# Performance work log

Measured on AMD Instinct MI355X. Metric: run time of the kernel, lower is better.

## Reference

```python
import jax, jax.numpy as jnp
import numpy as np

B, S, N, D, H = 4, 1024, 1024, 1024, 16
HD = D // H
EPS = 1e-5


def _xavier(key, shape):
    fan_in, fan_out = shape[1], shape[0]
    a = (6.0 / (fan_in + fan_out)) ** 0.5
    return jax.random.uniform(key, shape, jnp.float32, -a, a)


def layer_norm(x, g, b):
    m = jnp.mean(x, axis=-1, keepdims=True)
    v = jnp.mean(jnp.square(x - m), axis=-1, keepdims=True)
    return (x - m) * jax.lax.rsqrt(v + EPS) * g + b


def setup_inputs() -> dict:
    key = jax.random.key(0)
    ks = jax.random.split(key, 8)
    return {
        "x_q": jax.random.normal(ks[0], (B, S, D), jnp.float32),
        "x_k": jax.random.normal(ks[1], (B, N, D), jnp.float32),
        "x_v": jax.random.normal(ks[2], (B, N, D), jnp.float32),
        "Wq": _xavier(ks[3], (D, D)),
        "Wk": _xavier(ks[4], (D, D)),
        "Wv": _xavier(ks[5], (D, D)),
        "Wp": _xavier(ks[6], (D, D)),
        "qn_g": jnp.ones((HD,), jnp.float32),
        "qn_b": jnp.zeros((HD,), jnp.float32),
        "kn_g": jnp.ones((HD,), jnp.float32),
        "kn_b": jnp.zeros((HD,), jnp.float32),
        "on_g": jnp.ones((D,), jnp.float32),
        "on_b": jnp.zeros((D,), jnp.float32),
    }


def reference(x_q, x_k, x_v, Wq, Wk, Wv, Wp, qn_g, qn_b, kn_g, kn_b, on_g, on_b):
    scale = HD ** (-0.5)
    q = jnp.einsum('bsd,ed->bse', x_q, Wq)  # torch Linear: x @ W.T
    k = jnp.einsum('bnd,ed->bne', x_k, Wk)
    v = jnp.einsum('bnd,ed->bne', x_v, Wv)
    # Faithful to original: q is reshaped WITHOUT transpose (B,H,S,HD)
    q = q.reshape(B, H, S, HD)
    k = k.reshape(B, N, H, HD).transpose(0, 2, 1, 3)  # (B,H,N,HD)
    v = v.reshape(B, N, H, HD).transpose(0, 2, 1, 3)  # (B,H,N,HD)
    q = layer_norm(q, qn_g, qn_b) * scale
    k = layer_norm(k, kn_g, kn_b)
    attn = jax.nn.softmax(jnp.einsum('bhsd,bhnd->bhsn', q, k), axis=-1)
    x = jnp.einsum('bhsn,bhnd->bhsd', attn, v)
    x = x.transpose(0, 2, 1, 3).reshape(B, S, D)
    x = layer_norm(x, on_g, on_b)
    return jnp.einsum('bsd,ed->bse', x, Wp)
```

## Files before the change

kernel.cpp:

```cpp
#include <hip/hip_runtime.h>
#include <cstdint>

typedef unsigned short u16;
typedef __attribute__((ext_vector_type(4))) float f32x4;
typedef __attribute__((ext_vector_type(8))) short bf16x8;

__device__ __forceinline__ u16 f2bf(float f) {
  uint32_t u = __builtin_bit_cast(uint32_t, f);
  u += 0x7FFFu + ((u >> 16) & 1u);
  return (u16)(u >> 16);
}

__device__ __forceinline__ void gld16(const void* g, void* l) {
  __builtin_amdgcn_global_load_lds((const __attribute__((address_space(1))) void*)g,
                                   (__attribute__((address_space(3))) void*)l,
                                   16, 0, 0);
}

__global__ __launch_bounds__(256) void cast_all(const float* __restrict__ xq, const float* __restrict__ xk,
                                                const float* __restrict__ xv, const float* __restrict__ Wq,
                                                const float* __restrict__ Wk, const float* __restrict__ Wv,
                                                const float* __restrict__ Wp,
                                                u16* __restrict__ oq, u16* __restrict__ ok, u16* __restrict__ ov,
                                                u16* __restrict__ owq, u16* __restrict__ owk,
                                                u16* __restrict__ owv, u16* __restrict__ owp) {
  int bid = blockIdx.x;
  const float* src; u16* dst; size_t i;
  if (bid < 12288) {
    const int p = bid >> 12, ib = bid & 4095;
    src = (p == 0) ? xq : ((p == 1) ? xk : xv);
    dst = (p == 0) ? oq : ((p == 1) ? ok : ov);
    i = (size_t)ib * 256 + threadIdx.x;
  } else {
    bid -= 12288;
    const int p = bid >> 10, ib = bid & 1023;
    src = (p == 0) ? Wq : ((p == 1) ? Wk : ((p == 2) ? Wv : Wp));
    dst = (p == 0) ? owq : ((p == 1) ? owk : ((p == 2) ? owv : owp));
    i = (size_t)ib * 256 + threadIdx.x;
  }
  float4 v = *(const float4*)(src + i * 4);
  uint2 pk;
  pk.x = (uint32_t)f2bf(v.x) | ((uint32_t)f2bf(v.y) << 16);
  pk.y = (uint32_t)f2bf(v.z) | ((uint32_t)f2bf(v.w) << 16);
  *(uint2*)(dst + i * 4) = pk;
}

__device__ __forceinline__ void gemm_mainloop(const u16* __restrict__ A, const u16* __restrict__ B,
                                              int bm, int bn, u16* Al, u16* Bl,
                                              f32x4 (&acc)[4][4]) {
  const int t = threadIdx.x;
  const int w = t >> 6;
  const int lane = t & 63;
  const int l15 = lane & 15, l4 = lane >> 4;
  const int wr = w >> 1, wc = w & 1;

  const u16* Ab = A + (size_t)bm * 128 * 1024;
  const u16* Bb = B + (size_t)bn * 128 * 1024;

  for (int kt = 0; kt < 1024; kt += 64) {
#pragma unroll
    for (int p = 0; p < 4; ++p) {
      const int idx = p * 256 + t;
      const int row = idx >> 3, ch = idx & 7;
      const int sch = ch ^ (row & 7);
      gld16(Ab + (size_t)row * 1024 + kt + sch * 8, (char*)Al + p * 4096 + (w << 10));
      gld16(Bb + (size_t)row * 1024 + kt + sch * 8, (char*)Bl + p * 4096 + (w << 10));
    }
    __syncthreads();
#pragma unroll
    for (int ks = 0; ks < 2; ++ks) {
      bf16x8 af[4], bfr[4];
#pragma unroll
      for (int mi = 0; mi < 4; ++mi) {
        const int row = wr * 64 + mi * 16 + l15;
        const int ch = (ks * 4 + l4) ^ (row & 7);
        af[mi] = *(const bf16x8*)&Al[row * 64 + ch * 8];
      }
#pragma unroll
      for (int nj = 0; nj < 4; ++nj) {
        const int row = wc * 64 + nj * 16 + l15;
        const int ch = (ks * 4 + l4) ^ (row & 7);
        bfr[nj] = *(const bf16x8*)&Bl[row * 64 + ch * 8];
      }
#pragma unroll
      for (int mi = 0; mi < 4; ++mi)
#pragma unroll
        for (int nj = 0; nj < 4; ++nj)
          acc[mi][nj] = __builtin_amdgcn_mfma_f32_16x16x32_bf16(af[mi], bfr[nj], acc[mi][nj], 0, 0, 0);
    }
    __syncthreads();
  }
}

__global__ __launch_bounds__(256) void gemm_qkv(const u16* __restrict__ A0, const u16* __restrict__ A1,
                                                const u16* __restrict__ A2, const u16* __restrict__ B0,
                                                const u16* __restrict__ B1, const u16* __restrict__ B2,
                                                u16* __restrict__ Qout, u16* __restrict__ Kout,
                                                u16* __restrict__ Vout,
                                                const float* __restrict__ qg, const float* __restrict__ qb,
                                                const float* __restrict__ kg, const float* __restrict__ kb) {
  __shared__ __align__(16) u16 Al[128 * 64];
  __shared__ __align__(16) u16 Bl[128 * 64];
  const int p = blockIdx.x >> 8;
  const int b0 = blockIdx.x & 255;
  const int bid = ((b0 & 7) << 5) + (b0 >> 3);
  const int bm = bid >> 3, bn = bid & 7;
  const u16* A = (p == 0) ? A0 : ((p == 1) ? A1 : A2);
  const u16* B = (p == 0) ? B0 : ((p == 1) ? B1 : B2);

  f32x4 acc[4][4];
#pragma unroll
  for (int i = 0; i < 4; ++i)
#pragma unroll
    for (int j = 0; j < 4; ++j) acc[i][j] = (f32x4){0.f, 0.f, 0.f, 0.f};

  gemm_mainloop(A, B, bm, bn, Al, Bl, acc);

  const int t = threadIdx.x, w = t >> 6, lane = t & 63;
  const int l15 = lane & 15, l4 = lane >> 4;
  const int wr = w >> 1, wc = w & 1;
  const int c = bn * 2 + wc;

  if (p == 2) {
#pragma unroll
    for (int mi = 0; mi < 4; ++mi) {
      const int n0 = bm * 128 + wr * 64 + mi * 16 + l4 * 4;
      const int bi = n0 >> 10, ni = n0 & 1023;
      const int nt = ni >> 6, ng = (ni >> 3) & 7, no = ni & 7;
#pragma unroll
      for (int nj = 0; nj < 4; ++nj) {
        const int hd = nj * 16 + l15;
        uint32_t w0 = (uint32_t)f2bf(acc[mi][nj][0]) | ((uint32_t)f2bf(acc[mi][nj][1]) << 16);
        uint32_t w1 = (uint32_t)f2bf(acc[mi][nj][2]) | ((uint32_t)f2bf(acc[mi][nj][3]) << 16);
        uint2 pk = {w0, w1};
        const size_t addr = ((size_t)(bi * 16 + c) * 64 + hd) * 1024 + nt * 64 + ((ng ^ (hd & 7)) << 3) + no;
        *(uint2*)(Vout + addr) = pk;
      }
    }
    return;
  }

  const float scale = (p == 0) ? 0.18033688011112042f : 1.0f;
  const float* gv = (p == 0) ? qg : kg;
  const float* bv = (p == 0) ? qb : kb;
  u16* out = (p == 0) ? Qout : Kout;
  float gl[4], blc[4];
#pragma unroll
  for (int nj = 0; nj < 4; ++nj) {
    gl[nj] = gv[nj * 16 + l15];
    blc[nj] = bv[nj * 16 + l15] * scale;
  }
#pragma unroll
  for (int mi = 0; mi < 4; ++mi) {
#pragma unroll
    for (int r = 0; r < 4; ++r) {
      float s1 = 0.f, s2 = 0.f;
#pragma unroll
      for (int nj = 0; nj < 4; ++nj) {
        const float x = acc[mi][nj][r];
        s1 += x; s2 += x * x;
      }
#pragma unroll
      for (int mk = 1; mk < 16; mk <<= 1) {
        s1 += __shfl_xor(s1, mk, 64);
        s2 += __shfl_xor(s2, mk, 64);
      }
      const float mean = s1 * (1.0f / 64.0f);
      const float var = s2 * (1.0f / 64.0f) - mean * mean;
      const float rr = rsqrtf(var + 1e-5f) * scale;
      const int row_g = bm * 128 + wr * 64 + mi * 16 + l4 * 4 + r;
      const int bi = row_g >> 10, rsi = row_g & 1023;
      size_t base; int sw;
      if (p == 0) {
        const int h = rsi >> 6;
        const int s2i = ((rsi & 63) << 4) + c;
        base = ((size_t)(bi * 16 + h) * 1024 + s2i) * 64;
        sw = (s2i & 7) << 3;
      } else {
        base = ((size_t)(bi * 16 + c) * 1024 + rsi) * 64;
        sw = (rsi & 7) << 3;
      }
#pragma unroll
      for (int nj = 0; nj < 4; ++nj) {
        const float y = (acc[mi][nj][r] - mean) * rr * gl[nj] + blc[nj];
        out[base + ((nj * 16 + l15) ^ sw)] = f2bf(y);
      }
    }
  }
}

__global__ __launch_bounds__(256) void gemm_p(const u16* __restrict__ A, const u16* __restrict__ B,
                                              float* __restrict__ C) {
  __shared__ __align__(16) u16 Al[128 * 64];
  __shared__ __align__(16) u16 Bl[128 * 64];
  const int bid = ((blockIdx.x & 7) << 5) + (blockIdx.x >> 3);
  const int bm = bid >> 3, bn = bid & 7;

  f32x4 acc[4][4];
#pragma unroll
  for (int i = 0; i < 4; ++i)
#pragma unroll
    for (int j = 0; j < 4; ++j) acc[i][j] = (f32x4){0.f, 0.f, 0.f, 0.f};

  gemm_mainloop(A, B, bm, bn, Al, Bl, acc);

  const int t = threadIdx.x, w = t >> 6, lane = t & 63;
  const int l15 = lane & 15, l4 = lane >> 4;
  const int wr = w >> 1, wc = w & 1;
  float* Cb = C + (size_t)bm * 128 * 1024 + bn * 128;
#pragma unroll
  for (int mi = 0; mi < 4; ++mi)
#pragma unroll
    for (int nj = 0; nj < 4; ++nj) {
      const int row = wr * 64 + mi * 16 + l4 * 4;
      const int col = wc * 64 + nj * 16 + l15;
#pragma unroll
      for (int r = 0; r < 4; ++r)
        Cb[(size_t)(row + r) * 1024 + col] = acc[mi][nj][r];
    }
}

__global__ __launch_bounds__(256) void flash(const u16* __restrict__ Q,
                                             const u16* __restrict__ Km,
                                             const u16* __restrict__ Vt,
                                             float* __restrict__ ctx) {
  __shared__ __align__(16) u16 Kl[2 * 64 * 64];
  __shared__ __align__(16) u16 Vl[2 * 64 * 64];
  __shared__ __align__(16) u16 Pl[64 * 64];
  const int bid = ((blockIdx.x & 7) << 7) + (blockIdx.x >> 3);
  const int bh = bid >> 4, qt = bid & 15;
  const int t = threadIdx.x, w = t >> 6, lane = t & 63;
  const int l15 = lane & 15, l4 = lane >> 4;
  const int sx = (l15 & 7) << 3;
  const int ea0 = (l4 * 8) ^ sx;
  const int ea1 = ea0 ^ 32;

  const u16* Qrow = Q + ((size_t)bh * 1024 + qt * 64 + w * 16 + l15) * 64;
  const bf16x8 aq0 = *(const bf16x8*)(Qrow + ea0);
  const bf16x8 aq1 = *(const bf16x8*)(Qrow + ea1);
  const bf16x8 vone = {0x3F80, 0x3F80, 0x3F80, 0x3F80, 0x3F80, 0x3F80, 0x3F80, 0x3F80};

  const u16* Kg = Km + (size_t)bh * 65536;
  const u16* Vg = Vt + (size_t)bh * 65536;

  gld16((const char*)Kg + t * 16, (char*)Kl + (w << 10));
  gld16((const char*)Kg + 4096 + t * 16, (char*)Kl + 4096 + (w << 10));
  gld16(Vg + (t >> 3) * 1024 + (t & 7) * 8, (char*)Vl + (w << 10));
  gld16(Vg + ((t + 256) >> 3) * 1024 + (t & 7) * 8, (char*)Vl + 4096 + (w << 10));
  __syncthreads();

  f32x4 o[4];
  for (int i = 0; i < 4; ++i) o[i] = (f32x4){0.f, 0.f, 0.f, 0.f};
  f32x4 o4 = (f32x4){0.f, 0.f, 0.f, 0.f};

  int cur = 0;
  for (int nt2 = 0; nt2 < 16; ++nt2) {
    if (nt2 < 15) {
      const int nb = (cur ^ 1) * 8192;
      const char* ksrc = (const char*)(Kg + (size_t)(nt2 + 1) * 4096);
      gld16(ksrc + t * 16, (char*)Kl + nb + (w << 10));
      gld16(ksrc + 4096 + t * 16, (char*)Kl + nb + 4096 + (w << 10));
      gld16(Vg + (t >> 3) * 1024 + (nt2 + 1) * 64 + (t & 7) * 8, (char*)Vl + nb + (w << 10));
      gld16(Vg + ((t + 256) >> 3) * 1024 + (nt2 + 1) * 64 + (t & 7) * 8, (char*)Vl + nb + 4096 + (w << 10));
    }
    const u16* Kc = Kl + cur * 4096;
    const u16* Vc = Vl + cur * 4096;

    f32x4 sc[4];
    for (int cj = 0; cj < 4; ++cj) sc[cj] = (f32x4){0.f, 0.f, 0.f, 0.f};
#pragma unroll
    for (int ks = 0; ks < 2; ++ks) {
      const int ea = ks ? ea1 : ea0;
      const bf16x8 aq = ks ? aq1 : aq0;
#pragma unroll
      for (int cj = 0; cj < 4; ++cj) {
        bf16x8 bk = *(const bf16x8*)&Kc[(cj * 16 + l15) * 64 + ea];
        sc[cj] = __builtin_amdgcn_mfma_f32_16x16x32_bf16(aq, bk, sc[cj], 0, 0, 0);
      }
    }

#pragma unroll
    for (int cj = 0; cj < 4; ++cj)
#pragma unroll
      for (int r = 0; r < 4; ++r) {
        const float pf = __builtin_amdgcn_exp2f(sc[cj][r]);
        const uint32_t u = __builtin_bit_cast(uint32_t, pf);
        const int prow = w * 16 + l4 * 4 + r;
        Pl[prow * 64 + ((cj * 16 + l15) ^ (((l4 * 4 + r) & 7) << 3))] = (u16)((u + 0x8000u) >> 16);
      }

#pragma unroll
    for (int ks = 0; ks < 2; ++ks) {
      const int ea = ks ? ea1 : ea0;
      bf16x8 ap = *(const bf16x8*)&Pl[(w * 16 + l15) * 64 + ea];
#pragma unroll
      for (int c2 = 0; c2 < 4; ++c2) {
        bf16x8 bv = *(const bf16x8*)&Vc[(c2 * 16 + l15) * 64 + ea];
        o[c2] = __builtin_amdgcn_mfma_f32_16x16x32_bf16(ap, bv, o[c2], 0, 0, 0);
      }
      o4 = __builtin_amdgcn_mfma_f32_16x16x32_bf16(ap, vone, o4, 0, 0, 0);
    }
    __syncthreads();
    cur ^= 1;
  }

  const int b = bh >> 4, h = bh & 15;
#pragma unroll
  for (int c2 = 0; c2 < 4; ++c2) {
#pragma unroll
    for (int r = 0; r < 4; ++r) {
      const int s2 = qt * 64 + w * 16 + l4 * 4 + r;
      const int hd = c2 * 16 + l15;
      ctx[((size_t)b * 1024 + s2) * 1024 + h * 64 + hd] = o[c2][r] / o4[r];
    }
  }
}

__global__ __launch_bounds__(256) void ln_row(const float* __restrict__ X,
                                              const float* __restrict__ g,
                                              const float* __restrict__ bb,
                                              u16* __restrict__ out) {
  __shared__ float red[8];
  const int row = blockIdx.x, t = threadIdx.x;
  const int w = t >> 6, lane = t & 63;
  const float* xr = X + (size_t)row * 1024;
  float4 v = *(const float4*)(xr + t * 4);
  float s = v.x + v.y + v.z + v.w;
  for (int mk = 1; mk < 64; mk <<= 1) s += __shfl_xor(s, mk, 64);
  if (lane == 0) red[w] = s;
  __syncthreads();
  const float mean = (red[0] + red[1] + red[2] + red[3]) * (1.0f / 1024.0f);
  const float dx = v.x - mean, dy = v.y - mean, dz = v.z - mean, dw = v.w - mean;
  float q = dx * dx + dy * dy + dz * dz + dw * dw;
  for (int mk = 1; mk < 64; mk <<= 1) q += __shfl_xor(q, mk, 64);
  if (lane == 0) red[4 + w] = q;
  __syncthreads();
  const float var = (red[4] + red[5] + red[6] + red[7]) * (1.0f / 1024.0f);
  const float rs = rsqrtf(var + 1e-5f);
  float4 gg = *(const float4*)(g + t * 4);
  float4 b4 = *(const float4*)(bb + t * 4);
  uint2 pk;
  pk.x = (uint32_t)f2bf(dx * rs * gg.x + b4.x) | ((uint32_t)f2bf(dy * rs * gg.y + b4.y) << 16);
  pk.y = (uint32_t)f2bf(dz * rs * gg.z + b4.z) | ((uint32_t)f2bf(dw * rs * gg.w + b4.w) << 16);
  *(uint2*)(out + (size_t)row * 1024 + t * 4) = pk;
}

extern "C" void kernel_launch(void* const* d_in, const int* in_sizes, int n_in,
                              void* d_out, int out_size, void* d_ws, size_t ws_size,
                              hipStream_t stream) {
  (void)in_sizes; (void)n_in; (void)out_size; (void)ws_size;
  const float* x_q = (const float*)d_in[0];
  const float* x_k = (const float*)d_in[1];
  const float* x_v = (const float*)d_in[2];
  const float* Wq  = (const float*)d_in[3];
  const float* Wk  = (const float*)d_in[4];
  const float* Wv  = (const float*)d_in[5];
  const float* Wp  = (const float*)d_in[6];
  const float* qn_g = (const float*)d_in[7];
  const float* qn_b = (const float*)d_in[8];
  const float* kn_g = (const float*)d_in[9];
  const float* kn_b = (const float*)d_in[10];
  const float* on_g = (const float*)d_in[11];
  const float* on_b = (const float*)d_in[12];

  char* ws = (char*)d_ws;
  u16* xq_bf = (u16*)(ws + (0ull << 20));
  u16* xk_bf = (u16*)(ws + (8ull << 20));
  u16* xv_bf = (u16*)(ws + (16ull << 20));
  u16* Wq_bf = (u16*)(ws + (24ull << 20));
  u16* Wk_bf = (u16*)(ws + (26ull << 20));
  u16* Wv_bf = (u16*)(ws + (28ull << 20));
  u16* Wp_bf = (u16*)(ws + (30ull << 20));
  u16* Qa   = (u16*)(ws + (32ull << 20));
  u16* Ka   = (u16*)(ws + (40ull << 20));
  u16* Vtb  = (u16*)(ws + (48ull << 20));
  float* ctxf = (float*)(ws + (56ull << 20));
  u16* ctxb = (u16*)(ws + (72ull << 20));

  cast_all<<<16384, 256, 0, stream>>>(x_q, x_k, x_v, Wq, Wk, Wv, Wp,
                                      xq_bf, xk_bf, xv_bf, Wq_bf, Wk_bf, Wv_bf, Wp_bf);

  gemm_qkv<<<768, 256, 0, stream>>>(xq_bf, xk_bf, xv_bf, Wq_bf, Wk_bf, Wv_bf,
                                    Qa, Ka, Vtb, qn_g, qn_b, kn_g, kn_b);
  flash<<<1024, 256, 0, stream>>>(Qa, Ka, Vtb, ctxf);
  ln_row<<<4096, 256, 0, stream>>>(ctxf, on_g, on_b, ctxb);
  gemm_p<<<256, 256, 0, stream>>>(ctxb, Wp_bf, (float*)d_out);
}
```

Measured before the change: 126.9 us.

## Double-buffer GEMM K-loop in half tiles and process two query tiles per flash block

```diff
diff --git a/kernel.cpp b/kernel.cpp
--- a/kernel.cpp
+++ b/kernel.cpp
@@ -56,39 +56,60 @@
 
   const u16* Ab = A + (size_t)bm * 128 * 1024;
   const u16* Bb = B + (size_t)bn * 128 * 1024;
-
-  for (int kt = 0; kt < 1024; kt += 64) {
-#pragma unroll
-    for (int p = 0; p < 4; ++p) {
-      const int idx = p * 256 + t;
-      const int row = idx >> 3, ch = idx & 7;
-      const int sch = ch ^ (row & 7);
-      gld16(Ab + (size_t)row * 1024 + kt + sch * 8, (char*)Al + p * 4096 + (w << 10));
-      gld16(Bb + (size_t)row * 1024 + kt + sch * 8, (char*)Bl + p * 4096 + (w << 10));
-    }
-    __syncthreads();
-#pragma unroll
-    for (int ks = 0; ks < 2; ++ks) {
+  const int r0 = t >> 2, c0 = (t & 3) * 8;
+  const int r1 = r0 + 64;
+  const int wb = w << 10;
+
+  gld16(Ab + (size_t)r0 * 1024 + c0, (char*)Al + wb);
+  gld16(Ab + (size_t)r1 * 1024 + c0, (char*)Al + 4096 + wb);
+  gld16(Bb + (size_t)r0 * 1024 + c0, (char*)Bl + wb);
+  gld16(Bb + (size_t)r1 * 1024 + c0, (char*)Bl + 4096 + wb);
+  __syncthreads();
+
+#pragma unroll 1
+  for (int it = 0; it < 16; ++it) {
+    {
+      const int ktn = it * 64 + 32;
+      gld16(Ab + (size_t)r0 * 1024 + ktn + c0, (char*)Al + 8192 + wb);
+      gld16(Ab + (size_t)r1 * 1024 + ktn + c0, (char*)Al + 8192 + 4096 + wb);
+      gld16(Bb + (size_t)r0 * 1024 + ktn + c0, (char*)Bl + 8192 + wb);
+      gld16(Bb + (size_t)r1 * 1024 + ktn + c0, (char*)Bl + 8192 + 4096 + wb);
       bf16x8 af[4], bfr[4];
 #pragma unroll
-      for (int mi = 0; mi < 4; ++mi) {
-        const int row = wr * 64 + mi * 16 + l15;
-        const int ch = (ks * 4 + l4) ^ (row & 7);
-        af[mi] = *(const bf16x8*)&Al[row * 64 + ch * 8];
-      }
-#pragma unroll
-      for (int nj = 0; nj < 4; ++nj) {
-        const int row = wc * 64 + nj * 16 + l15;
-        const int ch = (ks * 4 + l4) ^ (row & 7);
-        bfr[nj] = *(const bf16x8*)&Bl[row * 64 + ch * 8];
-      }
+      for (int mi = 0; mi < 4; ++mi)
+        af[mi] = *(const bf16x8*)&Al[(wr * 64 + mi * 16 + l15) * 32 + l4 * 8];
+#pragma unroll
+      for (int nj = 0; nj < 4; ++nj)
+        bfr[nj] = *(const bf16x8*)&Bl[(wc * 64 + nj * 16 + l15) * 32 + l4 * 8];
 #pragma unroll
       for (int mi = 0; mi < 4; ++mi)
 #pragma unroll
         for (int nj = 0; nj < 4; ++nj)
           acc[mi][nj] = __builtin_amdgcn_mfma_f32_16x16x32_bf16(af[mi], bfr[nj], acc[mi][nj], 0, 0, 0);
-    }
-    __syncthreads();
+      __syncthreads();
+    }
+    {
+      const int ktn = it * 64 + 64;
+      if (ktn < 1024) {
+        gld16(Ab + (size_t)r0 * 1024 + ktn + c0, (char*)Al + wb);
+        gld16(Ab + (size_t)r1 * 1024 + ktn + c0, (char*)Al + 4096 + wb);
+        gld16(Bb + (size_t)r0 * 1024 + ktn + c0, (char*)Bl + wb);
+        gld16(Bb + (size_t)r1 * 1024 + ktn + c0, (char*)Bl + 4096 + wb);
+      }
+      bf16x8 af[4], bfr[4];
+#pragma unroll
+      for (int mi = 0; mi < 4; ++mi)
+        af[mi] = *(const bf16x8*)&Al[4096 + (wr * 64 + mi * 16 + l15) * 32 + l4 * 8];
+#pragma unroll
+      for (int nj = 0; nj < 4; ++nj)
+        bfr[nj] = *(const bf16x8*)&Bl[4096 + (wc * 64 + nj * 16 + l15) * 32 + l4 * 8];
+#pragma unroll
+      for (int mi = 0; mi < 4; ++mi)
+#pragma unroll
+        for (int nj = 0; nj < 4; ++nj)
+          acc[mi][nj] = __builtin_amdgcn_mfma_f32_16x16x32_bf16(af[mi], bfr[nj], acc[mi][nj], 0, 0, 0);
+      __syncthreads();
+    }
   }
 }
 
@@ -99,8 +120,8 @@
                                                 u16* __restrict__ Vout,
                                                 const float* __restrict__ qg, const float* __restrict__ qb,
                                                 const float* __restrict__ kg, const float* __restrict__ kb) {
-  __shared__ __align__(16) u16 Al[128 * 64];
-  __shared__ __align__(16) u16 Bl[128 * 64];
+  __shared__ __align__(16) u16 Al[2 * 128 * 32];
+  __shared__ __align__(16) u16 Bl[2 * 128 * 32];
   const int p = blockIdx.x >> 8;
   const int b0 = blockIdx.x & 255;
   const int bid = ((b0 & 7) << 5) + (b0 >> 3);
@@ -191,8 +212,8 @@
 
 __global__ __launch_bounds__(256) void gemm_p(const u16* __restrict__ A, const u16* __restrict__ B,
                                               float* __restrict__ C) {
-  __shared__ __align__(16) u16 Al[128 * 64];
-  __shared__ __align__(16) u16 Bl[128 * 64];
+  __shared__ __align__(16) u16 Al[2 * 128 * 32];
+  __shared__ __align__(16) u16 Bl[2 * 128 * 32];
   const int bid = ((blockIdx.x & 7) << 5) + (blockIdx.x >> 3);
   const int bm = bid >> 3, bn = bid & 7;
 
@@ -226,18 +247,20 @@
                                              float* __restrict__ ctx) {
   __shared__ __align__(16) u16 Kl[2 * 64 * 64];
   __shared__ __align__(16) u16 Vl[2 * 64 * 64];
-  __shared__ __align__(16) u16 Pl[64 * 64];
-  const int bid = ((blockIdx.x & 7) << 7) + (blockIdx.x >> 3);
-  const int bh = bid >> 4, qt = bid & 15;
+  __shared__ __align__(16) u16 Pl[2 * 64 * 64];
+  const int bid = ((blockIdx.x & 7) << 6) + (blockIdx.x >> 3);
+  const int bh = bid >> 3, qt2 = bid & 7;
   const int t = threadIdx.x, w = t >> 6, lane = t & 63;
   const int l15 = lane & 15, l4 = lane >> 4;
   const int sx = (l15 & 7) << 3;
   const int ea0 = (l4 * 8) ^ sx;
   const int ea1 = ea0 ^ 32;
 
-  const u16* Qrow = Q + ((size_t)bh * 1024 + qt * 64 + w * 16 + l15) * 64;
-  const bf16x8 aq0 = *(const bf16x8*)(Qrow + ea0);
-  const bf16x8 aq1 = *(const bf16x8*)(Qrow + ea1);
+  const u16* Qrow = Q + ((size_t)bh * 1024 + qt2 * 128 + w * 16 + l15) * 64;
+  const bf16x8 aq00 = *(const bf16x8*)(Qrow + ea0);
+  const bf16x8 aq01 = *(const bf16x8*)(Qrow + ea1);
+  const bf16x8 aq10 = *(const bf16x8*)(Qrow + 4096 + ea0);
+  const bf16x8 aq11 = *(const bf16x8*)(Qrow + 4096 + ea1);
   const bf16x8 vone = {0x3F80, 0x3F80, 0x3F80, 0x3F80, 0x3F80, 0x3F80, 0x3F80, 0x3F80};
 
   const u16* Kg = Km + (size_t)bh * 65536;
@@ -249,9 +272,13 @@
   gld16(Vg + ((t + 256) >> 3) * 1024 + (t & 7) * 8, (char*)Vl + 4096 + (w << 10));
   __syncthreads();
 
-  f32x4 o[4];
-  for (int i = 0; i < 4; ++i) o[i] = (f32x4){0.f, 0.f, 0.f, 0.f};
-  f32x4 o4 = (f32x4){0.f, 0.f, 0.f, 0.f};
+  f32x4 o[2][4];
+  f32x4 o4[2];
+#pragma unroll
+  for (int s = 0; s < 2; ++s) {
+    for (int i = 0; i < 4; ++i) o[s][i] = (f32x4){0.f, 0.f, 0.f, 0.f};
+    o4[s] = (f32x4){0.f, 0.f, 0.f, 0.f};
+  }
 
   int cur = 0;
   for (int nt2 = 0; nt2 < 16; ++nt2) {
@@ -266,39 +293,46 @@
     const u16* Kc = Kl + cur * 4096;
     const u16* Vc = Vl + cur * 4096;
 
-    f32x4 sc[4];
-    for (int cj = 0; cj < 4; ++cj) sc[cj] = (f32x4){0.f, 0.f, 0.f, 0.f};
-#pragma unroll
-    for (int ks = 0; ks < 2; ++ks) {
-      const int ea = ks ? ea1 : ea0;
-      const bf16x8 aq = ks ? aq1 : aq0;
-#pragma unroll
-      for (int cj = 0; cj < 4; ++cj) {
-        bf16x8 bk = *(const bf16x8*)&Kc[(cj * 16 + l15) * 64 + ea];
-        sc[cj] = __builtin_amdgcn_mfma_f32_16x16x32_bf16(aq, bk, sc[cj], 0, 0, 0);
-      }
-    }
-
-#pragma unroll
-    for (int cj = 0; cj < 4; ++cj)
-#pragma unroll
-      for (int r = 0; r < 4; ++r) {
-        const float pf = __builtin_amdgcn_exp2f(sc[cj][r]);
-        const uint32_t u = __builtin_bit_cast(uint32_t, pf);
-        const int prow = w * 16 + l4 * 4 + r;
-        Pl[prow * 64 + ((cj * 16 + l15) ^ (((l4 * 4 + r) & 7) << 3))] = (u16)((u + 0x8000u) >> 16);
-      }
-
-#pragma unroll
-    for (int ks = 0; ks < 2; ++ks) {
-      const int ea = ks ? ea1 : ea0;
-      bf16x8 ap = *(const bf16x8*)&Pl[(w * 16 + l15) * 64 + ea];
-#pragma unroll
-      for (int c2 = 0; c2 < 4; ++c2) {
-        bf16x8 bv = *(const bf16x8*)&Vc[(c2 * 16 + l15) * 64 + ea];
-        o[c2] = __builtin_amdgcn_mfma_f32_16x16x32_bf16(ap, bv, o[c2], 0, 0, 0);
-      }
-      o4 = __builtin_amdgcn_mfma_f32_16x16x32_bf16(ap, vone, o4, 0, 0, 0);
+#pragma unroll
+    for (int s = 0; s < 2; ++s) {
+      const bf16x8 aqa = s ? aq10 : aq00;
+      const bf16x8 aqb = s ? aq11 : aq01;
+      u16* Ps = Pl + s * 4096;
+
+      f32x4 sc[4];
+      for (int cj = 0; cj < 4; ++cj) sc[cj] = (f32x4){0.f, 0.f, 0.f, 0.f};
+#pragma unroll
+      for (int ks = 0; ks < 2; ++ks) {
+        const int ea = ks ? ea1 : ea0;
+        const bf16x8 aq = ks ? aqb : aqa;
+#pragma unroll
+        for (int cj = 0; cj < 4; ++cj) {
+          bf16x8 bk = *(const bf16x8*)&Kc[(cj * 16 + l15) * 64 + ea];
+          sc[cj] = __builtin_amdgcn_mfma_f32_16x16x32_bf16(aq, bk, sc[cj], 0, 0, 0);
+        }
+      }
+
+#pragma unroll
+      for (int cj = 0; cj < 4; ++cj)
+#pragma unroll
+        for (int r = 0; r < 4; ++r) {
+          const float pf = __builtin_amdgcn_exp2f(sc[cj][r]);
+          const uint32_t u = __builtin_bit_cast(uint32_t, pf);
+          const int prow = w * 16 + l4 * 4 + r;
+          Ps[prow * 64 + ((cj * 16 + l15) ^ (((l4 * 4 + r) & 7) << 3))] = (u16)((u + 0x8000u) >> 16);
+        }
+
+#pragma unroll
+      for (int ks = 0; ks < 2; ++ks) {
+        const int ea = ks ? ea1 : ea0;
+        bf16x8 ap = *(const bf16x8*)&Ps[(w * 16 + l15) * 64 + ea];
+#pragma unroll
+        for (int c2 = 0; c2 < 4; ++c2) {
+          bf16x8 bv = *(const bf16x8*)&Vc[(c2 * 16 + l15) * 64 + ea];
+          o[s][c2] = __builtin_amdgcn_mfma_f32_16x16x32_bf16(ap, bv, o[s][c2], 0, 0, 0);
+        }
+        o4[s] = __builtin_amdgcn_mfma_f32_16x16x32_bf16(ap, vone, o4[s], 0, 0, 0);
+      }
     }
     __syncthreads();
     cur ^= 1;
@@ -306,14 +340,16 @@
 
   const int b = bh >> 4, h = bh & 15;
 #pragma unroll
-  for (int c2 = 0; c2 < 4; ++c2) {
-#pragma unroll
-    for (int r = 0; r < 4; ++r) {
-      const int s2 = qt * 64 + w * 16 + l4 * 4 + r;
-      const int hd = c2 * 16 + l15;
-      ctx[((size_t)b * 1024 + s2) * 1024 + h * 64 + hd] = o[c2][r] / o4[r];
-    }
-  }
+  for (int s = 0; s < 2; ++s)
+#pragma unroll
+    for (int c2 = 0; c2 < 4; ++c2) {
+#pragma unroll
+      for (int r = 0; r < 4; ++r) {
+        const int s2 = qt2 * 128 + s * 64 + w * 16 + l4 * 4 + r;
+        const int hd = c2 * 16 + l15;
+        ctx[((size_t)b * 1024 + s2) * 1024 + h * 64 + hd] = o[s][c2][r] / o4[s][r];
+      }
+    }
 }
 
 __global__ __launch_bounds__(256) void ln_row(const float* __restrict__ X,
@@ -382,7 +418,7 @@
 
   gemm_qkv<<<768, 256, 0, stream>>>(xq_bf, xk_bf, xv_bf, Wq_bf, Wk_bf, Wv_bf,
                                     Qa, Ka, Vtb, qn_g, qn_b, kn_g, kn_b);
-  flash<<<1024, 256, 0, stream>>>(Qa, Ka, Vtb, ctxf);
+  flash<<<512, 256, 0, stream>>>(Qa, Ka, Vtb, ctxf);
   ln_row<<<4096, 256, 0, stream>>>(ctxf, on_g, on_b, ctxb);
   gemm_p<<<256, 256, 0, stream>>>(ctxb, Wp_bf, (float*)d_out);
 }
```

Measured after the change: 135.9 us. 1.07x slower.
